# Optimization experiments

Hardware: AMD Instinct MI355X
Metric: run time of the kernel (lower is better)

The kernel has to match this reference:

```python
import jax, jax.numpy as jnp
import numpy as np

B, DIM, H, W = 4, 96, 256, 256
HEADS = 4
EPS = 1e-12

def conv1x1(x, w, b):
    # x: [b,c,h,w], w: [o,c,1,1], b: [o]
    return jnp.einsum('bchw,oc->bohw', x, w[:, :, 0, 0]) + b[None, :, None, None]

def dwconv3x3(x, w, b):
    # depthwise 3x3, w: [c,1,3,3]
    c = x.shape[1]
    y = jax.lax.conv_general_dilated(
        x, w, window_strides=(1, 1), padding='SAME',
        feature_group_count=c, dimension_numbers=('NCHW', 'OIHW', 'NCHW'))
    return y + b[None, :, None, None]

def setup_inputs() -> dict:
    key = jax.random.key(0)
    ks = jax.random.split(key, 16)
    d = DIM
    s = 0.05
    return {
        'content': jax.random.normal(ks[0], (B, d, H, W), jnp.float32),
        'style': jax.random.normal(ks[1], (B, d, H, W), jnp.float32),
        'temperature': jnp.ones((HEADS, 1, 1), jnp.float32),
        'q_w': jax.random.normal(ks[2], (d, d, 1, 1), jnp.float32) * s,
        'q_b': jax.random.normal(ks[3], (d,), jnp.float32) * s,
        'qd_w': jax.random.normal(ks[4], (d, 1, 3, 3), jnp.float32) * s,
        'qd_b': jax.random.normal(ks[5], (d,), jnp.float32) * s,
        'kv_w': jax.random.normal(ks[6], (3 * d, d, 1, 1), jnp.float32) * s,
        'kv_b': jax.random.normal(ks[7], (3 * d,), jnp.float32) * s,
        'kvd_w': jax.random.normal(ks[8], (3 * d, 1, 3, 3), jnp.float32) * s,
        'kvd_b': jax.random.normal(ks[9], (3 * d,), jnp.float32) * s,
        'ps_w': jax.random.normal(ks[10], (d, d, 1, 1), jnp.float32) * s,
        'ps_b': jax.random.normal(ks[11], (d,), jnp.float32) * s,
        'psh_w': jax.random.normal(ks[12], (d, d, 1, 1), jnp.float32) * s,
        'psh_b': jax.random.normal(ks[13], (d,), jnp.float32) * s,
    }

def _heads(x, b, h, w):
    # [b, head*c, h, w] -> [b, head, c, h*w]
    return x.reshape(b, HEADS, x.shape[1] // HEADS, h * w)

def reference(content, style, temperature, q_w, q_b, qd_w, qd_b,
              kv_w, kv_b, kvd_w, kvd_b, ps_w, ps_b, psh_w, psh_b):
    b, c, h, w = content.shape
    kv = dwconv3x3(conv1x1(style, kv_w, kv_b), kvd_w, kvd_b)
    k, v_scale, v_shift = jnp.split(kv, 3, axis=1)
    q = dwconv3x3(conv1x1(content, q_w, q_b), qd_w, qd_b)

    q = _heads(q, b, h, w)
    k = _heads(k, b, h, w)
    v_scale = _heads(v_scale, b, h, w)
    v_shift = _heads(v_shift, b, h, w)

    # L2-normalize over spatial dim (torch F.normalize eps=1e-12)
    q = q / jnp.maximum(jnp.linalg.norm(q, axis=-1, keepdims=True), EPS)
    k = k / jnp.maximum(jnp.linalg.norm(k, axis=-1, keepdims=True), EPS)

    # attn: [b, head, c, c] (channel attention, tiny)
    attn = jnp.einsum('bhcn,bhdn->bhcd', q, k) * temperature[None]
    attn = jax.nn.softmax(attn, axis=-1)

    scale = jnp.einsum('bhcd,bhdn->bhcn', attn, v_scale).reshape(b, c, h, w)
    shift = jnp.einsum('bhcd,bhdn->bhcn', attn, v_shift).reshape(b, c, h, w)

    scale = conv1x1(scale, ps_w, ps_b)
    shift = conv1x1(shift, psh_w, psh_b)
    return (scale, shift)
```

## Files before the change

kernel.cpp:

```cpp
#include <hip/hip_runtime.h>

#define NB 4
#define C 96
#define HH 256
#define WW 256
#define NPIX (HH*WW)
#define HEADS 4
#define CH 24

#define NTX2 16
#define NTY2 19
#define NTILES (NTX2*NTY2)
#define YP 296
#define QP 264
#define VP 104
#define KSPLIT 128
#define YR 24
#define YC 392
#define XTP 76
#define VCH 40

#define WS_SUMSQ_Q 0
#define WS_SUMSQ_K (WS_SUMSQ_Q + NB*C)
#define WS_GRAM    (WS_SUMSQ_K + NB*C)
#define WS_MS      (WS_GRAM + NB*HEADS*CH*CH)
#define WS_MSH     (WS_MS + NB*C*C)

#define XT_OFF_BYTES ((size_t)335872)
#define XT_BYTES   ((size_t)2*NB*NPIX*96*2)

#define F_PSQ_OFF   (XT_OFF_BYTES + XT_BYTES)
#define F_PSQ_BYTES ((size_t)NTILES*NB*192*4)
#define F_PG_OFF    (F_PSQ_OFF + F_PSQ_BYTES)
#define F_PG_BYTES  ((size_t)NTILES*NB*HEADS*1024*4)
#define F_MB_OFF    (F_PG_OFF + F_PG_BYTES)
#define F_MB_BYTES  ((size_t)2*NB*96*96*2)
#define F_WS_NEED   (F_MB_OFF + F_MB_BYTES)

#define QK_OFF    (XT_OFF_BYTES + XT_BYTES)
#define QK_BYTES  ((size_t)2*NB*96*NPIX*2)
#define PG_OFF    (QK_OFF + QK_BYTES)
#define PG_BYTES  ((size_t)KSPLIT*NB*9216*4)
#define PSQ_OFF   (PG_OFF + PG_BYTES)
#define PSQ_BYTES ((size_t)4*NTILES*NB*48*4)
#define MB_OFF    (PSQ_OFF + PSQ_BYTES)
#define MB_BYTES  ((size_t)2*NB*96*96*2)
#define WB_OFF    (MB_OFF + MB_BYTES)
#define WB_BYTES  ((size_t)384*96*2)
#define WS_NEED3  (WB_OFF + WB_BYTES)

typedef short short8 __attribute__((ext_vector_type(8)));
typedef float f32x4 __attribute__((ext_vector_type(4)));
typedef float f32x16 __attribute__((ext_vector_type(16)));

__device__ __forceinline__ unsigned short f2b(float f){
  unsigned u = __float_as_uint(f);
  unsigned r = u + 0x7FFFu + ((u >> 16) & 1u);
  return (unsigned short)(r >> 16);
}
__device__ __forceinline__ float b2f(unsigned short s){
  return __uint_as_float(((unsigned)s) << 16);
}
__device__ __forceinline__ unsigned cvtpk(float lo, float hi){
  unsigned r;
  asm("v_cvt_pk_bf16_f32 %0, %1, %2" : "=v"(r) : "v"(lo), "v"(hi));
  return r;
}
__device__ __forceinline__ short8 pack8(float4 a, float4 b){
  short8 r;
  r[0]=(short)f2b(a.x); r[1]=(short)f2b(a.y); r[2]=(short)f2b(a.z); r[3]=(short)f2b(a.w);
  r[4]=(short)f2b(b.x); r[5]=(short)f2b(b.y); r[6]=(short)f2b(b.z); r[7]=(short)f2b(b.w);
  return r;
}

__global__ __launch_bounds__(256) void k0t(
  const float* __restrict__ content, const float* __restrict__ style,
  unsigned short* __restrict__ xt, int cm)
{
  __shared__ unsigned short Xt[96*XTP];
  const int t = threadIdx.x;
  const int n0 = blockIdx.x * 64;
  const int b = blockIdx.y, src = blockIdx.z;
  const int gyr = n0 >> 8, gxb = n0 & 255;
  const float* in = (src ? style : content) + (size_t)b*C*NPIX;
  #pragma unroll
  for (int i = 0; i < 6; ++i){
    int s = i*256 + t;
    int r = s >> 4, c4 = s & 15;
    float4 f = *(const float4*)(in + (size_t)r*NPIX + n0 + c4*4);
    unsigned lo = ((unsigned)f2b(f.y) << 16) | f2b(f.x);
    unsigned hi = ((unsigned)f2b(f.w) << 16) | f2b(f.z);
    *(uint2*)&Xt[r*XTP + c4*4] = make_uint2(lo, hi);
  }
  __syncthreads();
  unsigned* dst = (unsigned*)(xt + ((size_t)src*NB + b)*NPIX*96);
  #pragma unroll
  for (int i = 0; i < 12; ++i){
    int s = i*256 + t;
    int j = s / 48, c2 = s - j*48;
    unsigned v = ((unsigned)Xt[(c2*2+1)*XTP + j] << 16) | Xt[(c2*2)*XTP + j];
    size_t np = cm ? ((size_t)(gxb + j)*HH + gyr) : (size_t)(n0 + j);
    dst[np*48 + c2] = v;
  }
}

__global__ __launch_bounds__(256) void kwpack(
  const float* __restrict__ q_w, const float* __restrict__ kv_w,
  unsigned short* __restrict__ wb)
{
  int i = blockIdx.x*256 + threadIdx.x;
  if (i < 9216) wb[i] = f2b(q_w[i]);
  else if (i < 36864) wb[i] = f2b(kv_w[i - 9216]);
}

__global__ __launch_bounds__(512, 4) void kconv(
  const unsigned short* __restrict__ xt, const unsigned short* __restrict__ wb,
  const float* __restrict__ q_b, const float* __restrict__ qd_w, const float* __restrict__ qd_b,
  const float* __restrict__ kv_b, const float* __restrict__ kvd_w, const float* __restrict__ kvd_b,
  unsigned short* __restrict__ qk, float* __restrict__ psq)
{
  __shared__ unsigned short Ysh[48*YC];
  __shared__ float red[48];
  const int t = threadIdx.x, lane = t & 63, w = t >> 6;
  const int tile = blockIdx.x, b = blockIdx.y, z = blockIdx.z;
  const int txx = tile & 15, tyy = tile >> 4;
  const int gx0 = txx*16, gy0 = tyy*14;
  const unsigned short* xsrc = xt + ((size_t)((z < 2 ? 0 : 1)*NB + b))*NPIX*96;
  const int wrow0 = (z < 2) ? z*48 : 96 + (z-2)*48;
  const float* cb  = (z<2) ? q_b  + z*48           : kv_b  + (size_t)(z-2)*48;
  const float* dww = (z<2) ? qd_w + (size_t)z*48*9 : kvd_w + (size_t)(z-2)*48*9;
  const float* dwb = (z<2) ? qd_b + z*48           : kvd_b + (size_t)(z-2)*48;
  unsigned short* dst0 = (z < 2)
      ? qk + ((size_t)(0*NB + b)*96 + (size_t)z*48)*NPIX
      : qk + ((size_t)(1*NB + b)*96 + (size_t)(z-2)*48)*NPIX;

  if (t < 48) red[t] = 0.f;

  const int hy = lane & 15, khalf = lane >> 4;
  const int gyh = gy0 - 1 + hy;
  short8 xf[3][3]; bool imv[3];
  const int np = (w < 2) ? 3 : 2;
  #pragma unroll
  for (int i = 0; i < 3; ++i){
    if (i >= np) break;
    int pt = w + i*8;
    int gx = gx0 - 1 + pt;
    bool im = (gx>=0) && (gx<WW) && (gyh>=0) && (gyh<HH);
    imv[i] = im;
    const unsigned short* xp = xsrc + (size_t)(im ? (gx*HH + gyh) : 0)*96 + khalf*8;
    short8 zz = {};
    #pragma unroll
    for (int kk = 0; kk < 3; ++kk){
      short8 v = *(const short8*)(xp + kk*32);
      xf[i][kk] = im ? v : zz;
    }
  }

  #pragma unroll 1
  for (int mi = 0; mi < 3; ++mi){
    const unsigned short* wp = wb + (size_t)(wrow0 + mi*16 + hy)*96 + khalf*8;
    short8 a0 = *(const short8*)(wp);
    short8 a1 = *(const short8*)(wp + 32);
    short8 a2 = *(const short8*)(wp + 64);
    float4 bv = *(const float4*)&cb[mi*16 + khalf*4];
    #pragma unroll
    for (int i = 0; i < 3; ++i){
      if (i >= np) break;
      int pt = w + i*8;
      f32x4 acc = {bv.x, bv.y, bv.z, bv.w};
      acc = __builtin_amdgcn_mfma_f32_16x16x32_bf16(a0, xf[i][0], acc, 0,0,0);
      acc = __builtin_amdgcn_mfma_f32_16x16x32_bf16(a1, xf[i][1], acc, 0,0,0);
      acc = __builtin_amdgcn_mfma_f32_16x16x32_bf16(a2, xf[i][2], acc, 0,0,0);
      #pragma unroll
      for (int r = 0; r < 4; ++r){
        int ch = mi*16 + khalf*4 + r;
        Ysh[ch*YC + hy*YR + pt] = imv[i] ? f2b(acc[r]) : (unsigned short)0;
      }
    }
  }
  __syncthreads();

  for (int sl = lane; sl < 84; sl += 64){
    int slot = w*84 + sl;
    int c = slot / 14, py = slot - (slot/14)*14;
    int gy = gy0 + py;
    if (gy < HH){
      const float* wd = dww + (size_t)c*9;
      float w00=wd[0],w01=wd[1],w02=wd[2],w10=wd[3],w11=wd[4],w12=wd[5],w20=wd[6],w21=wd[7],w22=wd[8];
      float bb = dwb[c];
      const unsigned short* yb = &Ysh[c*YC + py*YR];
      float o[16];
      #pragma unroll
      for (int half = 0; half < 2; ++half){
        float u[3][10];
        #pragma unroll
        for (int uu = 0; uu < 3; ++uu){
          const unsigned short* rp = yb + uu*YR + half*8;
          short8 s = *(const short8*)rp;
          unsigned ex = *(const unsigned*)(rp + 8);
          #pragma unroll
          for (int j = 0; j < 8; ++j) u[uu][j] = b2f((unsigned short)s[j]);
          u[uu][8] = b2f((unsigned short)(ex & 0xffffu));
          u[uu][9] = b2f((unsigned short)(ex >> 16));
        }
        #pragma unroll
        for (int j = 0; j < 8; ++j){
          float s = bb;
          s = fmaf(w00,u[0][j],s); s = fmaf(w01,u[0][j+1],s); s = fmaf(w02,u[0][j+2],s);
          s = fmaf(w10,u[1][j],s); s = fmaf(w11,u[1][j+1],s); s = fmaf(w12,u[1][j+2],s);
          s = fmaf(w20,u[2][j],s); s = fmaf(w21,u[2][j+1],s); s = fmaf(w22,u[2][j+2],s);
          o[half*8 + j] = s;
        }
      }
      float sq = 0.f;
      #pragma unroll
      for (int j = 0; j < 16; ++j) sq = fmaf(o[j], o[j], sq);
      atomicAdd(&red[c], sq);
      unsigned vvp[8];
      #pragma unroll
      for (int jj = 0; jj < 8; ++jj) vvp[jj] = cvtpk(o[2*jj], o[2*jj+1]);
      unsigned short* qp = dst0 + (size_t)c*NPIX + (size_t)gy*WW + gx0;
      *(uint4*)qp       = make_uint4(vvp[0], vvp[1], vvp[2], vvp[3]);
      *(uint4*)(qp + 8) = make_uint4(vvp[4], vvp[5], vvp[6], vvp[7]);
    }
  }
  __syncthreads();
  if (t < 48)
    psq[((size_t)(z*NTILES + tile)*NB + b)*48 + t] = red[t];
}

__global__ __launch_bounds__(384) void kgram(
  const unsigned short* __restrict__ qk, float* __restrict__ pg)
{
  const int t = threadIdx.x, lane = t & 63, wv = t >> 6;
  const int ks = blockIdx.x, b = blockIdx.y;
  const int n0 = ks * (NPIX / KSPLIT);
  const unsigned short* qb = qk + ((size_t)(0*NB + b)*96)*NPIX;
  const unsigned short* kb = qk + ((size_t)(1*NB + b)*96)*NPIX;
  f32x4 acc[6];
  #pragma unroll
  for (int i = 0; i < 6; ++i) acc[i] = (f32x4){0.f,0.f,0.f,0.f};
  #pragma unroll 1
  for (int st = 0; st < (NPIX/KSPLIT)/32; ++st){
    int off = n0 + st*32 + (lane>>4)*8;
    short8 bf = *(const short8*)(kb + (size_t)(wv*16 + (lane&15))*NPIX + off);
    #pragma unroll
    for (int ci = 0; ci < 6; ++ci){
      short8 af = *(const short8*)(qb + (size_t)(ci*16 + (lane&15))*NPIX + off);
      acc[ci] = __builtin_amdgcn_mfma_f32_16x16x32_bf16(af, bf, acc[ci], 0,0,0);
    }
  }
  float* dst = pg + ((size_t)ks*NB + b)*9216;
  #pragma unroll
  for (int ci = 0; ci < 6; ++ci){
    #pragma unroll
    for (int r = 0; r < 4; ++r)
      dst[(ci*6 + wv)*256 + ((lane>>4)*4 + r)*16 + (lane&15)] = acc[ci][r];
  }
}

__global__ __launch_bounds__(256) void kgredN(
  const float* __restrict__ pg, const float* __restrict__ psq, float* __restrict__ ws)
{
  const int b = blockIdx.x, by = blockIdx.y, t = threadIdx.x;
  if (by < 36){
    int ci = by / 6;
    int qrow = ci*16 + (t >> 4), krow = (by - ci*6)*16 + (t & 15);
    float s = 0.f;
    for (int ks = 0; ks < KSPLIT; ++ks)
      s += pg[((size_t)ks*NB + b)*9216 + by*256 + t];
    int h = qrow / CH;
    if (krow / CH == h)
      ws[WS_GRAM + ((size_t)(b*HEADS + h)*CH + (qrow % CH))*CH + (krow % CH)] = s;
  } else {
    if (t < 192){
      int src = t / 96, c = t - (t/96)*96;
      int zz = src*2 + (c/48), cc = c - (c/48)*48;
      float s = 0.f;
      for (int tile = 0; tile < NTILES; ++tile)
        s += psq[((size_t)(zz*NTILES + tile)*NB + b)*48 + cc];
      ws[(src ? WS_SUMSQ_K : WS_SUMSQ_Q) + b*C + c] = s;
    }
  }
}

__global__ void k2_attn(
  const float* __restrict__ temp,
  const float* __restrict__ ps_w, const float* __restrict__ psh_w,
  float* __restrict__ ws, unsigned short* __restrict__ mb)
{
  const int b = blockIdx.x;
  const int t = threadIdx.x;
  __shared__ float attn[C * CH];
  __shared__ float nq[C], nk[C];
  if (t < C){
    nq[t] = fmaxf(sqrtf(ws[WS_SUMSQ_Q + b * C + t]), 1e-12f);
    nk[t] = fmaxf(sqrtf(ws[WS_SUMSQ_K + b * C + t]), 1e-12f);
  }
  __syncthreads();
  if (t < C){
    int h = t / CH;
    const float* g = ws + WS_GRAM + (((size_t)b * HEADS + h) * CH + (t % CH)) * CH;
    float tp = temp[h];
    float row[CH];
    float mx = -3.4e38f;
    #pragma unroll
    for (int d = 0; d < CH; ++d){
      row[d] = g[d] / (nq[t] * nk[h * CH + d]) * tp;
      mx = fmaxf(mx, row[d]);
    }
    float s = 0.f;
    #pragma unroll
    for (int d = 0; d < CH; ++d){ row[d] = expf(row[d] - mx); s += row[d]; }
    float inv = 1.f / s;
    #pragma unroll
    for (int d = 0; d < CH; ++d) attn[t * CH + d] = row[d] * inv;
  }
  __syncthreads();
  for (int idx = t; idx < C * C; idx += 256){
    int o = idx / C, dg = idx - o * C;
    int h = dg / CH, d = dg - h * CH;
    float s1 = 0.f, s2 = 0.f;
    #pragma unroll
    for (int c2 = 0; c2 < CH; ++c2){
      float a = attn[(h * CH + c2) * CH + d];
      s1 = fmaf(ps_w [(size_t)o * C + h * CH + c2], a, s1);
      s2 = fmaf(psh_w[(size_t)o * C + h * CH + c2], a, s2);
    }
    ws[WS_MS  + (size_t)b * C * C + idx] = s1;
    ws[WS_MSH + (size_t)b * C * C + idx] = s2;
    if (mb){
      mb[((size_t)0*NB + b)*9216 + idx] = f2b(s1);
      mb[((size_t)1*NB + b)*9216 + idx] = f2b(s2);
    }
  }
}

__global__ __launch_bounds__(512, 4) void kvm(
  const unsigned short* __restrict__ xt, const unsigned short* __restrict__ wb,
  const float* __restrict__ kv_b, const float* __restrict__ kvd_w, const float* __restrict__ kvd_b,
  const unsigned short* __restrict__ mb,
  const float* __restrict__ ps_b, const float* __restrict__ psh_b,
  float* __restrict__ out)
{
  __shared__ unsigned short Ysh[32*YC];
  __shared__ unsigned short vS[224*VCH];
  const int t = threadIdx.x, lane = t & 63, w = t >> 6;
  const int tile = blockIdx.x, b = blockIdx.y, z = blockIdx.z;
  const int txx = tile & 15, tyy = tile >> 4;
  const int gx0 = txx*16, gy0 = tyy*14;
  const unsigned short* xsrc = xt + ((size_t)(NB + b))*NPIX*96;

  const int hy = lane & 15, khalf = lane >> 4;
  const int gyh = gy0 - 1 + hy;
  short8 xf[3][3]; bool imv[3];
  const int np = (w < 2) ? 3 : 2;
  #pragma unroll
  for (int i = 0; i < 3; ++i){
    if (i >= np) break;
    int pt = w + i*8;
    int gx = gx0 - 1 + pt;
    bool im = (gx>=0) && (gx<WW) && (gyh>=0) && (gyh<HH);
    imv[i] = im;
    const unsigned short* xp = xsrc + (size_t)(im ? (gx*HH + gyh) : 0)*96 + khalf*8;
    short8 zz = {};
    #pragma unroll
    for (int kk = 0; kk < 3; ++kk){
      short8 v = *(const short8*)(xp + kk*32);
      xf[i][kk] = im ? v : zz;
    }
  }

  const float* bias = z ? psh_b : ps_b;
  f32x4 acc[6][2];
  #pragma unroll
  for (int mi = 0; mi < 6; ++mi){
    float4 bv = *(const float4*)&bias[mi*16 + khalf*4];
    acc[mi][0] = (f32x4){bv.x, bv.y, bv.z, bv.w};
    acc[mi][1] = acc[mi][0];
  }
  const unsigned short* mbp = mb + ((size_t)z*NB + b)*9216;

  #pragma unroll 1
  for (int ck = 0; ck < 3; ++ck){
    const int kvrow0 = 96 + z*96 + ck*32;
    #pragma unroll 1
    for (int mi2 = 0; mi2 < 2; ++mi2){
      const unsigned short* wp = wb + (size_t)(96 + kvrow0 + mi2*16 + hy)*96 + khalf*8;
      short8 a0 = *(const short8*)(wp);
      short8 a1 = *(const short8*)(wp + 32);
      short8 a2 = *(const short8*)(wp + 64);
      float4 bv = *(const float4*)&kv_b[kvrow0 + mi2*16 + khalf*4];
      #pragma unroll
      for (int i = 0; i < 3; ++i){
        if (i >= np) break;
        int pt = w + i*8;
        f32x4 a = {bv.x, bv.y, bv.z, bv.w};
        a = __builtin_amdgcn_mfma_f32_16x16x32_bf16(a0, xf[i][0], a, 0,0,0);
        a = __builtin_amdgcn_mfma_f32_16x16x32_bf16(a1, xf[i][1], a, 0,0,0);
        a = __builtin_amdgcn_mfma_f32_16x16x32_bf16(a2, xf[i][2], a, 0,0,0);
        #pragma unroll
        for (int r = 0; r < 4; ++r){
          int ch = mi2*16 + khalf*4 + r;
          Ysh[ch*YC + hy*YR + pt] = imv[i] ? f2b(a[r]) : (unsigned short)0;
        }
      }
    }
    __syncthreads();
    if (t < 448){
      int c2 = t & 31, py = t >> 5;
      const float* wd = kvd_w + (size_t)(kvrow0 + c2)*9;
      float w00=wd[0],w01=wd[1],w02=wd[2],w10=wd[3],w11=wd[4],w12=wd[5],w20=wd[6],w21=wd[7],w22=wd[8];
      float bb = kvd_b[kvrow0 + c2];
      const unsigned short* yb = &Ysh[c2*YC + py*YR];
      float o[16];
      #pragma unroll
      for (int half = 0; half < 2; ++half){
        float u[3][10];
        #pragma unroll
        for (int uu = 0; uu < 3; ++uu){
          const unsigned short* rp = yb + uu*YR + half*8;
          short8 s = *(const short8*)rp;
          unsigned ex = *(const unsigned*)(rp + 8);
          #pragma unroll
          for (int j = 0; j < 8; ++j) u[uu][j] = b2f((unsigned short)s[j]);
          u[uu][8] = b2f((unsigned short)(ex & 0xffffu));
          u[uu][9] = b2f((unsigned short)(ex >> 16));
        }
        #pragma unroll
        for (int j = 0; j < 8; ++j){
          float s = bb;
          s = fmaf(w00,u[0][j],s); s = fmaf(w01,u[0][j+1],s); s = fmaf(w02,u[0][j+2],s);
          s = fmaf(w10,u[1][j],s); s = fmaf(w11,u[1][j+1],s); s = fmaf(w12,u[1][j+2],s);
          s = fmaf(w20,u[2][j],s); s = fmaf(w21,u[2][j+1],s); s = fmaf(w22,u[2][j+2],s);
          o[half*8 + j] = s;
        }
      }
      #pragma unroll
      for (int jj = 0; jj < 8; ++jj){
        unsigned p = cvtpk(o[2*jj], o[2*jj+1]);
        vS[(py*16 + 2*jj    )*VCH + c2] = (unsigned short)p;
        vS[(py*16 + 2*jj + 1)*VCH + c2] = (unsigned short)(p >> 16);
      }
    }
    __syncthreads();
    #pragma unroll
    for (int mi = 0; mi < 6; ++mi){
      short8 a = *(const short8*)(mbp + (size_t)(mi*16 + hy)*96 + ck*32 + khalf*8);
      #pragma unroll
      for (int gi = 0; gi < 2; ++gi){
        int g = w + gi*8;
        if (g < 14){
          short8 bf = *(const short8*)&vS[(size_t)(g*16 + hy)*VCH + khalf*8];
          acc[mi][gi] = __builtin_amdgcn_mfma_f32_16x16x32_bf16(a, bf, acc[mi][gi], 0,0,0);
        }
      }
    }
    __syncthreads();
  }

  float* ob = out + ((size_t)z*NB + b)*(size_t)C*NPIX;
  #pragma unroll
  for (int gi = 0; gi < 2; ++gi){
    int g = w + gi*8;
    int gy = gy0 + g;
    if (g < 14 && gy < HH){
      #pragma unroll
      for (int mi = 0; mi < 6; ++mi){
        #pragma unroll
        for (int r = 0; r < 4; ++r)
          ob[(size_t)(mi*16 + khalf*4 + r)*NPIX + (size_t)gy*WW + gx0 + hy] = acc[mi][gi][r];
      }
    }
  }
}

__device__ __forceinline__ void conv48c(
  const unsigned short* __restrict__ xbase, const float* __restrict__ wmat,
  const float* __restrict__ bias, int row0,
  int gx0, int gy0, int lane, int w, unsigned short* __restrict__ Ysh)
{
  const int hy = lane & 15, khalf = lane >> 4;
  const int gy = gy0 - 1 + hy;
  short8 xf[3][3]; bool imv[3]; int np = (w < 2) ? 3 : 2;
  #pragma unroll
  for (int i = 0; i < 3; ++i){
    if (i >= np) break;
    int pt = w + i*8;
    int gx = gx0 - 1 + pt;
    bool im = (gx>=0) && (gx<WW) && (gy>=0) && (gy<HH);
    imv[i] = im;
    int n = im ? (gy*WW + gx) : 0;
    const unsigned short* xp = xbase + (size_t)n*96 + khalf*8;
    short8 z = {};
    #pragma unroll
    for (int kk = 0; kk < 3; ++kk){
      short8 v = *(const short8*)(xp + kk*32);
      xf[i][kk] = im ? v : z;
    }
  }
  #pragma unroll 1
  for (int mi = 0; mi < 3; ++mi){
    int orow = row0 + mi*16 + hy;
    const float* wp = wmat + (size_t)orow*96 + khalf*8;
    short8 a0 = pack8(*(const float4*)(wp),    *(const float4*)(wp+4));
    short8 a1 = pack8(*(const float4*)(wp+32), *(const float4*)(wp+36));
    short8 a2 = pack8(*(const float4*)(wp+64), *(const float4*)(wp+68));
    float4 bv = *(const float4*)&bias[row0 + mi*16 + khalf*4];
    #pragma unroll
    for (int i = 0; i < 3; ++i){
      if (i >= np) break;
      int pt = w + i*8;
      f32x4 acc = {bv.x, bv.y, bv.z, bv.w};
      acc = __builtin_amdgcn_mfma_f32_16x16x32_bf16(a0, xf[i][0], acc, 0,0,0);
      acc = __builtin_amdgcn_mfma_f32_16x16x32_bf16(a1, xf[i][1], acc, 0,0,0);
      acc = __builtin_amdgcn_mfma_f32_16x16x32_bf16(a2, xf[i][2], acc, 0,0,0);
      #pragma unroll
      for (int r = 0; r < 4; ++r){
        int ch = mi*16 + khalf*4 + r;
        Ysh[ch*YP + pt*16 + hy] = imv[i] ? f2b(acc[r]) : (unsigned short)0;
      }
    }
  }
}

__global__ __launch_bounds__(512, 4) void kqk(
  const unsigned short* __restrict__ xt,
  const float* __restrict__ q_w, const float* __restrict__ q_b,
  const float* __restrict__ qd_w, const float* __restrict__ qd_b,
  const float* __restrict__ kv_w, const float* __restrict__ kv_b,
  const float* __restrict__ kvd_w, const float* __restrict__ kvd_b,
  float* __restrict__ pg, float* __restrict__ psq)
{
  __shared__ unsigned short Ysh[48*YP];
  __shared__ unsigned short qS[48*QP];
  __shared__ unsigned short kT[48*QP];
  __shared__ float redq[C], redk[C];

  const int t = threadIdx.x, lane = t & 63, w = t >> 6;
  const int b = blockIdx.y, tile = blockIdx.x;
  const int txx = tile & 15, tyy = tile >> 4;
  const int gx0 = txx*16, gy0 = tyy*14;
  if (t < C){ redq[t] = 0.f; redk[t] = 0.f; }
  __syncthreads();

  const unsigned short* xc = xt + ((size_t)(0*NB + b))*NPIX*96;
  const unsigned short* xs = xt + ((size_t)(1*NB + b))*NPIX*96;

  auto dwQK = [&](const float* dww, const float* dwb, int wrow0,
                  unsigned short* dst, float* red){
    for (int slot = t; slot < 48*16; slot += 512){
      int c = slot >> 4, j = slot & 15;
      const unsigned short* yb = &Ysh[c*YP + j*16];
      float u0[16], u1[16], u2[16];
      {
        short8 s0 = *(const short8*)(yb),    short8_t_dummy = {};
        short8 s1 = *(const short8*)(yb+8);
        short8 s2 = *(const short8*)(yb+16), s3 = *(const short8*)(yb+24);
        short8 s4 = *(const short8*)(yb+32), s5 = *(const short8*)(yb+40);
        (void)short8_t_dummy;
        #pragma unroll
        for (int u = 0; u < 8; ++u){
          u0[u]=b2f((unsigned short)s0[u]); u0[u+8]=b2f((unsigned short)s1[u]);
          u1[u]=b2f((unsigned short)s2[u]); u1[u+8]=b2f((unsigned short)s3[u]);
          u2[u]=b2f((unsigned short)s4[u]); u2[u+8]=b2f((unsigned short)s5[u]);
        }
      }
      const float* wd = dww + (size_t)(wrow0 + c)*9;
      float w00=wd[0],w01=wd[1],w02=wd[2],w10=wd[3],w11=wd[4],w12=wd[5],w20=wd[6],w21=wd[7],w22=wd[8];
      float bb = dwb[wrow0 + c];
      unsigned short vv[16];
      float sq = 0.f;
      #pragma unroll
      for (int py = 0; py < 14; ++py){
        float s = bb;
        s = fmaf(w00,u0[py],s); s = fmaf(w10,u0[py+1],s); s = fmaf(w20,u0[py+2],s);
        s = fmaf(w01,u1[py],s); s = fmaf(w11,u1[py+1],s); s = fmaf(w21,u1[py+2],s);
        s = fmaf(w02,u2[py],s); s = fmaf(w12,u2[py+1],s); s = fmaf(w22,u2[py+2],s);
        if (gy0 + py >= HH) s = 0.f;
        sq = fmaf(s, s, sq);
        vv[py] = f2b(s);
      }
      vv[14] = 0; vv[15] = 0;
      atomicAdd(&red[wrow0 + c], sq);
      *(short8*)&dst[c*QP + j*16]     = *(short8*)&vv[0];
      *(short8*)&dst[c*QP + j*16 + 8] = *(short8*)&vv[8];
    }
  };

  auto gram = [&](int cc){
    int hl = w & 1, slice = w >> 1;
    int cl = lane & 31; bool cv = cl < CH;
    int row = hl*CH + (cv ? cl : 0);
    f32x16 g;
    #pragma unroll
    for (int r = 0; r < 16; ++r) g[r] = 0.f;
    short8 z = {};
    for (int ks = slice; ks < 16; ks += 4){
      int ko = ks*16 + (lane>>5)*8;
      short8 qa = *(const short8*)&qS[row*QP + ko];
      short8 kb = *(const short8*)&kT[row*QP + ko];
      if (!cv){ qa = z; kb = z; }
      g = __builtin_amdgcn_mfma_f32_32x32x16_bf16(qa, kb, g, 0,0,0);
    }
    float* stg = (float*)Ysh;
    if (slice != 0){
      float* dst = stg + (size_t)(hl*3 + slice - 1)*1024;
      #pragma unroll
      for (int r = 0; r < 16; ++r) dst[r*64 + lane] = g[r];
    }
    __syncthreads();
    if (slice == 0){
      const float* s0 = stg + (size_t)(hl*3 + 0)*1024;
      const float* s1 = stg + (size_t)(hl*3 + 1)*1024;
      const float* s2 = stg + (size_t)(hl*3 + 2)*1024;
      float* dst = pg + ((size_t)(tile*NB + b)*HEADS + cc*2 + hl)*1024;
      #pragma unroll
      for (int r = 0; r < 16; ++r){
        int ix = r*64 + lane;
        dst[ix] = g[r] + s0[ix] + s1[ix] + s2[ix];
      }
    }
  };

  #pragma unroll 1
  for (int cc = 0; cc < 2; ++cc){
    conv48c(xc, q_w, q_b, cc*48, gx0, gy0, lane, w, Ysh);
    __syncthreads();
    dwQK(qd_w, qd_b, cc*48, qS, redq);
    __syncthreads();
    conv48c(xs, kv_w, kv_b, cc*48, gx0, gy0, lane, w, Ysh);
    __syncthreads();
    dwQK(kvd_w, kvd_b, cc*48, kT, redk);
    __syncthreads();
    gram(cc);
    __syncthreads();
  }
  if (t < 192){
    float v = (t < 96) ? redq[t] : redk[t - 96];
    psq[(size_t)(tile*NB + b)*192 + t] = v;
  }
}

__global__ __launch_bounds__(256) void kgredF(
  const float* __restrict__ pg, const float* __restrict__ psq, float* __restrict__ ws)
{
  const int bh = blockIdx.x;
  const int b = bh >> 2, h = bh & 3;
  const int t = threadIdx.x;
  float a0=0.f, a1=0.f, a2=0.f, a3=0.f, sq=0.f;
  for (int tile = 0; tile < NTILES; ++tile){
    const float* p = pg + ((size_t)(tile*NB + b)*HEADS + h)*1024;
    a0 += p[t]; a1 += p[t+256]; a2 += p[t+512]; a3 += p[t+768];
    if (t < 48){
      int ch = h*CH + (t % CH);
      sq += psq[(size_t)(tile*NB + b)*192 + (t < CH ? ch : 96 + ch)];
    }
  }
  if (t < 48){
    if (t < CH) ws[WS_SUMSQ_Q + b*C + h*CH + t] = sq;
    else        ws[WS_SUMSQ_K + b*C + h*CH + (t - CH)] = sq;
  }
  float accs[4] = {a0, a1, a2, a3};
  #pragma unroll
  for (int i = 0; i < 4; ++i){
    int idx = i*256 + t;
    int r = idx >> 6, ln = idx & 63;
    int row = (r&3) + 8*(r>>2) + 4*(ln>>5);
    int col = ln & 31;
    if (row < CH && col < CH)
      ws[WS_GRAM + ((size_t)(b*HEADS + h)*CH + row)*CH + col] = accs[i];
  }
}

__global__ __launch_bounds__(512, 4) void kv_out(
  const unsigned short* __restrict__ xs,
  const float* __restrict__ kv_w, const float* __restrict__ kv_b,
  const float* __restrict__ kvd_w, const float* __restrict__ kvd_b,
  const float* __restrict__ ps_b, const float* __restrict__ psh_b,
  const unsigned short* __restrict__ mb, float* __restrict__ out)
{
  __shared__ unsigned short Ysh[48*YP];
  __shared__ unsigned short vS2[224*VP];
  const int t = threadIdx.x, lane = t & 63, w = t >> 6;
  const int b = blockIdx.y, tile = blockIdx.x;
  const int txx = tile & 15, tyy = tile >> 4;
  const int gx0 = txx*16, gy0 = tyy*14;
  const unsigned short* xb_ = xs + (size_t)b*NPIX*96;

  #pragma unroll 1
  for (int which = 0; which < 2; ++which){
    #pragma unroll 1
    for (int cv = 0; cv < 2; ++cv){
      int row0 = 96 + which*96 + cv*48;
      conv48c(xb_, kv_w, kv_b, row0, gx0, gy0, lane, w, Ysh);
      __syncthreads();
      for (int slot = t; slot < 48*16; slot += 512){
        int c = slot >> 4, j = slot & 15;
        const unsigned short* yb = &Ysh[c*YP + j*16];
        float u0[16], u1[16], u2[16];
        {
          short8 s0 = *(const short8*)(yb),    s1 = *(const short8*)(yb+8);
          short8 s2 = *(const short8*)(yb+16), s3 = *(const short8*)(yb+24);
          short8 s4 = *(const short8*)(yb+32), s5 = *(const short8*)(yb+40);
          #pragma unroll
          for (int u = 0; u < 8; ++u){
            u0[u]=b2f((unsigned short)s0[u]); u0[u+8]=b2f((unsigned short)s1[u]);
            u1[u]=b2f((unsigned short)s2[u]); u1[u+8]=b2f((unsigned short)s3[u]);
            u2[u]=b2f((unsigned short)s4[u]); u2[u+8]=b2f((unsigned short)s5[u]);
          }
        }
        const float* wd = kvd_w + (size_t)(row0 + c)*9;
        float w00=wd[0],w01=wd[1],w02=wd[2],w10=wd[3],w11=wd[4],w12=wd[5],w20=wd[6],w21=wd[7],w22=wd[8];
        float bb = kvd_b[row0 + c];
        #pragma unroll
        for (int py = 0; py < 14; ++py){
          float s = bb;
          s = fmaf(w00,u0[py],s); s = fmaf(w10,u0[py+1],s); s = fmaf(w20,u0[py+2],s);
          s = fmaf(w01,u1[py],s); s = fmaf(w11,u1[py+1],s); s = fmaf(w21,u1[py+2],s);
          s = fmaf(w02,u2[py],s); s = fmaf(w12,u2[py+1],s); s = fmaf(w22,u2[py+2],s);
          vS2[(py*16 + j)*VP + cv*48 + c] = f2b(s);
        }
      }
      __syncthreads();
    }
    const unsigned short* mbp = mb + ((size_t)which*NB + b)*9216;
    const float* bias = which ? psh_b : ps_b;
    float* ob = out + (size_t)which*NB*C*NPIX + (size_t)b*C*NPIX;
    for (int tl = w; tl < 84; tl += 8){
      int mi = tl / 14, n = tl - mi*14;
      const unsigned short* mp = mbp + (size_t)(mi*16 + (lane&15))*96 + (lane>>4)*8;
      short8 a0 = *(const short8*)(mp);
      short8 a1 = *(const short8*)(mp + 32);
      short8 a2 = *(const short8*)(mp + 64);
      float4 bv = *(const float4*)&bias[mi*16 + (lane>>4)*4];
      f32x4 acc = {bv.x, bv.y, bv.z, bv.w};
      const unsigned short* xb = &vS2[(size_t)(n*16 + (lane&15))*VP + (lane>>4)*8];
      acc = __builtin_amdgcn_mfma_f32_16x16x32_bf16(a0, *(const short8*)(xb),    acc, 0,0,0);
      acc = __builtin_amdgcn_mfma_f32_16x16x32_bf16(a1, *(const short8*)(xb+32), acc, 0,0,0);
      acc = __builtin_amdgcn_mfma_f32_16x16x32_bf16(a2, *(const short8*)(xb+64), acc, 0,0,0);
      int gy = gy0 + n;
      if (gy < HH){
        #pragma unroll
        for (int r = 0; r < 4; ++r)
          ob[(size_t)(mi*16 + (lane>>4)*4 + r)*NPIX + gy*WW + gx0 + (lane&15)] = acc[r];
      }
    }
    __syncthreads();
  }
}

extern "C" void kernel_launch(void* const* d_in, const int* in_sizes, int n_in,
                              void* d_out, int out_size, void* d_ws, size_t ws_size,
                              hipStream_t stream)
{
  const float* content = (const float*)d_in[0];
  const float* style   = (const float*)d_in[1];
  const float* temp    = (const float*)d_in[2];
  const float* q_w   = (const float*)d_in[3];
  const float* q_b   = (const float*)d_in[4];
  const float* qd_w  = (const float*)d_in[5];
  const float* qd_b  = (const float*)d_in[6];
  const float* kv_w  = (const float*)d_in[7];
  const float* kv_b  = (const float*)d_in[8];
  const float* kvd_w = (const float*)d_in[9];
  const float* kvd_b = (const float*)d_in[10];
  const float* ps_w  = (const float*)d_in[11];
  const float* ps_b  = (const float*)d_in[12];
  const float* psh_w = (const float*)d_in[13];
  const float* psh_b = (const float*)d_in[14];
  float* out = (float*)d_out;
  float* ws  = (float*)d_ws;

  unsigned short* xt = (unsigned short*)((char*)d_ws + XT_OFF_BYTES);

  if (ws_size >= WS_NEED3){
    unsigned short* qk  = (unsigned short*)((char*)d_ws + QK_OFF);
    float* pg  = (float*)((char*)d_ws + PG_OFF);
    float* psq = (float*)((char*)d_ws + PSQ_OFF);
    unsigned short* mb = (unsigned short*)((char*)d_ws + MB_OFF);
    unsigned short* wb = (unsigned short*)((char*)d_ws + WB_OFF);

    k0t<<<dim3(NPIX/64, NB, 2), dim3(256), 0, stream>>>(content, style, xt, 1);
    kwpack<<<dim3(144), dim3(256), 0, stream>>>(q_w, kv_w, wb);
    kconv<<<dim3(NTILES, NB, 4), dim3(512), 0, stream>>>(
        xt, wb, q_b, qd_w, qd_b, kv_b, kvd_w, kvd_b, qk, psq);
    kgram<<<dim3(KSPLIT, NB), dim3(384), 0, stream>>>(qk, pg);
    kgredN<<<dim3(NB, 37), dim3(256), 0, stream>>>(pg, psq, ws);
    k2_attn<<<dim3(NB), dim3(256), 0, stream>>>(temp, ps_w, psh_w, ws, mb);
    kvm<<<dim3(NTILES, NB, 2), dim3(512), 0, stream>>>(
        xt, wb, kv_b, kvd_w, kvd_b, mb, ps_b, psh_b, out);
  } else {
    float* pg  = (float*)((char*)d_ws + F_PG_OFF);
    float* psq = (float*)((char*)d_ws + F_PSQ_OFF);
    unsigned short* mb = (unsigned short*)((char*)d_ws + F_MB_OFF);
    k0t<<<dim3(NPIX/64, NB, 2), dim3(256), 0, stream>>>(content, style, xt, 0);
    kqk<<<dim3(NTILES, NB), dim3(512), 0, stream>>>(
        xt, q_w, q_b, qd_w, qd_b, kv_w, kv_b, kvd_w, kvd_b, pg, psq);
    kgredF<<<dim3(NB*HEADS), dim3(256), 0, stream>>>(pg, psq, ws);
    k2_attn<<<dim3(NB), dim3(256), 0, stream>>>(temp, ps_w, psh_w, ws, mb);
    kv_out<<<dim3(NTILES, NB), dim3(512), 0, stream>>>(
        xt + (size_t)NB*NPIX*96, kv_w, kv_b, kvd_w, kvd_b, ps_b, psh_b, mb, out);
  }
}
```

Measured before the change: 449.1 us.

## Store q/k in tile-major padded layout and remap blocks across XCDs

kconv now writes q/k intermediates in a tile-contiguous padded layout (224 pixels per tile, zeros for rows outside the image), so each row of 16 pixels lands contiguously and kgram streams a dense padded pixel range with a new split count. Both kconv and kvm also remap the flat block index so consecutive blocks are spread in strides of eight, a swizzle aimed at XCD/L2 locality. The intent is to cut scattered write traffic and improve cache locality, in exchange for a slightly larger qk buffer and gram work over padding pixels.

```diff
diff --git a/kernel.cpp b/kernel.cpp
--- a/kernel.cpp
+++ b/kernel.cpp
@@ -11,6 +11,9 @@
 #define NTX2 16
 #define NTY2 19
 #define NTILES (NTX2*NTY2)
+#define TPX 224
+#define NPIXP (NTILES*TPX)
+#define KSPL2 133
 #define YP 296
 #define QP 264
 #define VP 104
@@ -38,9 +41,9 @@
 #define F_WS_NEED   (F_MB_OFF + F_MB_BYTES)
 
 #define QK_OFF    (XT_OFF_BYTES + XT_BYTES)
-#define QK_BYTES  ((size_t)2*NB*96*NPIX*2)
+#define QK_BYTES  ((size_t)2*NB*96*NPIXP*2)
 #define PG_OFF    (QK_OFF + QK_BYTES)
-#define PG_BYTES  ((size_t)KSPLIT*NB*9216*4)
+#define PG_BYTES  ((size_t)KSPL2*NB*9216*4)
 #define PSQ_OFF   (PG_OFF + PG_BYTES)
 #define PSQ_BYTES ((size_t)4*NTILES*NB*48*4)
 #define MB_OFF    (PSQ_OFF + PSQ_BYTES)
@@ -122,7 +125,9 @@
   __shared__ unsigned short Ysh[48*YC];
   __shared__ float red[48];
   const int t = threadIdx.x, lane = t & 63, w = t >> 6;
-  const int tile = blockIdx.x, b = blockIdx.y, z = blockIdx.z;
+  const int F = blockIdx.x + NTILES*(blockIdx.y + NB*blockIdx.z);
+  const int W = (F & 7)*(NTILES*NB*4/8) + (F >> 3);
+  const int tile = W % NTILES, b = (W / NTILES) % NB, z = W / (NTILES*NB);
   const int txx = tile & 15, tyy = tile >> 4;
   const int gx0 = txx*16, gy0 = tyy*14;
   const unsigned short* xsrc = xt + ((size_t)((z < 2 ? 0 : 1)*NB + b))*NPIX*96;
@@ -131,8 +136,8 @@
   const float* dww = (z<2) ? qd_w + (size_t)z*48*9 : kvd_w + (size_t)(z-2)*48*9;
   const float* dwb = (z<2) ? qd_b + z*48           : kvd_b + (size_t)(z-2)*48;
   unsigned short* dst0 = (z < 2)
-      ? qk + ((size_t)(0*NB + b)*96 + (size_t)z*48)*NPIX
-      : qk + ((size_t)(1*NB + b)*96 + (size_t)(z-2)*48)*NPIX;
+      ? qk + ((size_t)(0*NB + b)*96 + (size_t)z*48)*NPIXP
+      : qk + ((size_t)(1*NB + b)*96 + (size_t)(z-2)*48)*NPIXP;
 
   if (t < 48) red[t] = 0.f;
 
@@ -184,11 +189,236 @@
     int slot = w*84 + sl;
     int c = slot / 14, py = slot - (slot/14)*14;
     int gy = gy0 + py;
-    if (gy < HH){
-      const float* wd = dww + (size_t)c*9;
+    bool valid = (gy < HH);
+    const float* wd = dww + (size_t)c*9;
+    float w00=wd[0],w01=wd[1],w02=wd[2],w10=wd[3],w11=wd[4],w12=wd[5],w20=wd[6],w21=wd[7],w22=wd[8];
+    float bb = dwb[c];
+    const unsigned short* yb = &Ysh[c*YC + py*YR];
+    float o[16];
+    #pragma unroll
+    for (int half = 0; half < 2; ++half){
+      float u[3][10];
+      #pragma unroll
+      for (int uu = 0; uu < 3; ++uu){
+        const unsigned short* rp = yb + uu*YR + half*8;
+        short8 s = *(const short8*)rp;
+        unsigned ex = *(const unsigned*)(rp + 8);
+        #pragma unroll
+        for (int j = 0; j < 8; ++j) u[uu][j] = b2f((unsigned short)s[j]);
+        u[uu][8] = b2f((unsigned short)(ex & 0xffffu));
+        u[uu][9] = b2f((unsigned short)(ex >> 16));
+      }
+      #pragma unroll
+      for (int j = 0; j < 8; ++j){
+        float s = bb;
+        s = fmaf(w00,u[0][j],s); s = fmaf(w01,u[0][j+1],s); s = fmaf(w02,u[0][j+2],s);
+        s = fmaf(w10,u[1][j],s); s = fmaf(w11,u[1][j+1],s); s = fmaf(w12,u[1][j+2],s);
+        s = fmaf(w20,u[2][j],s); s = fmaf(w21,u[2][j+1],s); s = fmaf(w22,u[2][j+2],s);
+        o[half*8 + j] = valid ? s : 0.f;
+      }
+    }
+    float sq = 0.f;
+    #pragma unroll
+    for (int j = 0; j < 16; ++j) sq = fmaf(o[j], o[j], sq);
+    atomicAdd(&red[c], sq);
+    unsigned vvp[8];
+    #pragma unroll
+    for (int jj = 0; jj < 8; ++jj) vvp[jj] = cvtpk(o[2*jj], o[2*jj+1]);
+    unsigned short* qp = dst0 + (size_t)c*NPIXP + tile*TPX + py*16;
+    *(uint4*)qp       = make_uint4(vvp[0], vvp[1], vvp[2], vvp[3]);
+    *(uint4*)(qp + 8) = make_uint4(vvp[4], vvp[5], vvp[6], vvp[7]);
+  }
+  __syncthreads();
+  if (t < 48)
+    psq[((size_t)(z*NTILES + tile)*NB + b)*48 + t] = red[t];
+}
+
+__global__ __launch_bounds__(384) void kgram(
+  const unsigned short* __restrict__ qk, float* __restrict__ pg)
+{
+  const int t = threadIdx.x, lane = t & 63, wv = t >> 6;
+  const int ks = blockIdx.x, b = blockIdx.y;
+  const int n0 = ks * 512;
+  const unsigned short* qb = qk + ((size_t)(0*NB + b)*96)*NPIXP;
+  const unsigned short* kb = qk + ((size_t)(1*NB + b)*96)*NPIXP;
+  f32x4 acc[6];
+  #pragma unroll
+  for (int i = 0; i < 6; ++i) acc[i] = (f32x4){0.f,0.f,0.f,0.f};
+  #pragma unroll 1
+  for (int st = 0; st < 16; ++st){
+    int off = n0 + st*32 + (lane>>4)*8;
+    short8 bf = *(const short8*)(kb + (size_t)(wv*16 + (lane&15))*NPIXP + off);
+    #pragma unroll
+    for (int ci = 0; ci < 6; ++ci){
+      short8 af = *(const short8*)(qb + (size_t)(ci*16 + (lane&15))*NPIXP + off);
+      acc[ci] = __builtin_amdgcn_mfma_f32_16x16x32_bf16(af, bf, acc[ci], 0,0,0);
+    }
+  }
+  float* dst = pg + ((size_t)ks*NB + b)*9216;
+  #pragma unroll
+  for (int ci = 0; ci < 6; ++ci){
+    #pragma unroll
+    for (int r = 0; r < 4; ++r)
+      dst[(ci*6 + wv)*256 + ((lane>>4)*4 + r)*16 + (lane&15)] = acc[ci][r];
+  }
+}
+
+__global__ __launch_bounds__(256) void kgredN(
+  const float* __restrict__ pg, const float* __restrict__ psq, float* __restrict__ ws)
+{
+  const int b = blockIdx.x, by = blockIdx.y, t = threadIdx.x;
+  if (by < 36){
+    int ci = by / 6;
+    int qrow = ci*16 + (t >> 4), krow = (by - ci*6)*16 + (t & 15);
+    float s = 0.f;
+    for (int ks = 0; ks < KSPL2; ++ks)
+      s += pg[((size_t)ks*NB + b)*9216 + by*256 + t];
+    int h = qrow / CH;
+    if (krow / CH == h)
+      ws[WS_GRAM + ((size_t)(b*HEADS + h)*CH + (qrow % CH))*CH + (krow % CH)] = s;
+  } else {
+    if (t < 192){
+      int src = t / 96, c = t - (t/96)*96;
+      int zz = src*2 + (c/48), cc = c - (c/48)*48;
+      float s = 0.f;
+      for (int tile = 0; tile < NTILES; ++tile)
+        s += psq[((size_t)(zz*NTILES + tile)*NB + b)*48 + cc];
+      ws[(src ? WS_SUMSQ_K : WS_SUMSQ_Q) + b*C + c] = s;
+    }
+  }
+}
+
+__global__ void k2_attn(
+  const float* __restrict__ temp,
+  const float* __restrict__ ps_w, const float* __restrict__ psh_w,
+  float* __restrict__ ws, unsigned short* __restrict__ mb)
+{
+  const int b = blockIdx.x;
+  const int t = threadIdx.x;
+  __shared__ float attn[C * CH];
+  __shared__ float nq[C], nk[C];
+  if (t < C){
+    nq[t] = fmaxf(sqrtf(ws[WS_SUMSQ_Q + b * C + t]), 1e-12f);
+    nk[t] = fmaxf(sqrtf(ws[WS_SUMSQ_K + b * C + t]), 1e-12f);
+  }
+  __syncthreads();
+  if (t < C){
+    int h = t / CH;
+    const float* g = ws + WS_GRAM + (((size_t)b * HEADS + h) * CH + (t % CH)) * CH;
+    float tp = temp[h];
+    float row[CH];
+    float mx = -3.4e38f;
+    #pragma unroll
+    for (int d = 0; d < CH; ++d){
+      row[d] = g[d] / (nq[t] * nk[h * CH + d]) * tp;
+      mx = fmaxf(mx, row[d]);
+    }
+    float s = 0.f;
+    #pragma unroll
+    for (int d = 0; d < CH; ++d){ row[d] = expf(row[d] - mx); s += row[d]; }
+    float inv = 1.f / s;
+    #pragma unroll
+    for (int d = 0; d < CH; ++d) attn[t * CH + d] = row[d] * inv;
+  }
+  __syncthreads();
+  for (int idx = t; idx < C * C; idx += 256){
+    int o = idx / C, dg = idx - o * C;
+    int h = dg / CH, d = dg - h * CH;
+    float s1 = 0.f, s2 = 0.f;
+    #pragma unroll
+    for (int c2 = 0; c2 < CH; ++c2){
+      float a = attn[(h * CH + c2) * CH + d];
+      s1 = fmaf(ps_w [(size_t)o * C + h * CH + c2], a, s1);
+      s2 = fmaf(psh_w[(size_t)o * C + h * CH + c2], a, s2);
+    }
+    ws[WS_MS  + (size_t)b * C * C + idx] = s1;
+    ws[WS_MSH + (size_t)b * C * C + idx] = s2;
+    if (mb){
+      mb[((size_t)0*NB + b)*9216 + idx] = f2b(s1);
+      mb[((size_t)1*NB + b)*9216 + idx] = f2b(s2);
+    }
+  }
+}
+
+__global__ __launch_bounds__(512, 4) void kvm(
+  const unsigned short* __restrict__ xt, const unsigned short* __restrict__ wb,
+  const float* __restrict__ kv_b, const float* __restrict__ kvd_w, const float* __restrict__ kvd_b,
+  const unsigned short* __restrict__ mb,
+  const float* __restrict__ ps_b, const float* __restrict__ psh_b,
+  float* __restrict__ out)
+{
+  __shared__ unsigned short Ysh[32*YC];
+  __shared__ unsigned short vS[224*VCH];
+  const int t = threadIdx.x, lane = t & 63, w = t >> 6;
+  const int F = blockIdx.x + NTILES*(blockIdx.y + NB*blockIdx.z);
+  const int W = (F & 7)*(NTILES*NB*2/8) + (F >> 3);
+  const int tile = W % NTILES, b = (W / NTILES) % NB, z = W / (NTILES*NB);
+  const int txx = tile & 15, tyy = tile >> 4;
+  const int gx0 = txx*16, gy0 = tyy*14;
+  const unsigned short* xsrc = xt + ((size_t)(NB + b))*NPIX*96;
+
+  const int hy = lane & 15, khalf = lane >> 4;
+  const int gyh = gy0 - 1 + hy;
+  short8 xf[3][3]; bool imv[3];
+  const int np = (w < 2) ? 3 : 2;
+  #pragma unroll
+  for (int i = 0; i < 3; ++i){
+    if (i >= np) break;
+    int pt = w + i*8;
+    int gx = gx0 - 1 + pt;
+    bool im = (gx>=0) && (gx<WW) && (gyh>=0) && (gyh<HH);
+    imv[i] = im;
+    const unsigned short* xp = xsrc + (size_t)(im ? (gx*HH + gyh) : 0)*96 + khalf*8;
+    short8 zz = {};
+    #pragma unroll
+    for (int kk = 0; kk < 3; ++kk){
+      short8 v = *(const short8*)(xp + kk*32);
+      xf[i][kk] = im ? v : zz;
+    }
+  }
+
+  const float* bias = z ? psh_b : ps_b;
+  f32x4 acc[6][2];
+  #pragma unroll
+  for (int mi = 0; mi < 6; ++mi){
+    float4 bv = *(const float4*)&bias[mi*16 + khalf*4];
+    acc[mi][0] = (f32x4){bv.x, bv.y, bv.z, bv.w};
+    acc[mi][1] = acc[mi][0];
+  }
+  const unsigned short* mbp = mb + ((size_t)z*NB + b)*9216;
+
+  #pragma unroll 1
+  for (int ck = 0; ck < 3; ++ck){
+    const int kvrow0 = 96 + z*96 + ck*32;
+    #pragma unroll 1
+    for (int mi2 = 0; mi2 < 2; ++mi2){
+      const unsigned short* wp = wb + (size_t)(96 + kvrow0 + mi2*16 + hy)*96 + khalf*8;
+      short8 a0 = *(const short8*)(wp);
+      short8 a1 = *(const short8*)(wp + 32);
+      short8 a2 = *(const short8*)(wp + 64);
+      float4 bv = *(const float4*)&kv_b[kvrow0 + mi2*16 + khalf*4];
+      #pragma unroll
+      for (int i = 0; i < 3; ++i){
+        if (i >= np) break;
+        int pt = w + i*8;
+        f32x4 a = {bv.x, bv.y, bv.z, bv.w};
+        a = __builtin_amdgcn_mfma_f32_16x16x32_bf16(a0, xf[i][0], a, 0,0,0);
+        a = __builtin_amdgcn_mfma_f32_16x16x32_bf16(a1, xf[i][1], a, 0,0,0);
+        a = __builtin_amdgcn_mfma_f32_16x16x32_bf16(a2, xf[i][2], a, 0,0,0);
+        #pragma unroll
+        for (int r = 0; r < 4; ++r){
+          int ch = mi2*16 + khalf*4 + r;
+          Ysh[ch*YC + hy*YR + pt] = imv[i] ? f2b(a[r]) : (unsigned short)0;
+        }
+      }
+    }
+    __syncthreads();
+    if (t < 448){
+      int c2 = t & 31, py = t >> 5;
+      const float* wd = kvd_w + (size_t)(kvrow0 + c2)*9;
       float w00=wd[0],w01=wd[1],w02=wd[2],w10=wd[3],w11=wd[4],w12=wd[5],w20=wd[6],w21=wd[7],w22=wd[8];
-      float bb = dwb[c];
-      const unsigned short* yb = &Ysh[c*YC + py*YR];
+      float bb = kvd_b[kvrow0 + c2];
+      const unsigned short* yb = &Ysh[c2*YC + py*YR];
       float o[16];
       #pragma unroll
       for (int half = 0; half < 2; ++half){
@@ -212,230 +442,6 @@
           o[half*8 + j] = s;
         }
       }
-      float sq = 0.f;
-      #pragma unroll
-      for (int j = 0; j < 16; ++j) sq = fmaf(o[j], o[j], sq);
-      atomicAdd(&red[c], sq);
-      unsigned vvp[8];
-      #pragma unroll
-      for (int jj = 0; jj < 8; ++jj) vvp[jj] = cvtpk(o[2*jj], o[2*jj+1]);
-      unsigned short* qp = dst0 + (size_t)c*NPIX + (size_t)gy*WW + gx0;
-      *(uint4*)qp       = make_uint4(vvp[0], vvp[1], vvp[2], vvp[3]);
-      *(uint4*)(qp + 8) = make_uint4(vvp[4], vvp[5], vvp[6], vvp[7]);
-    }
-  }
-  __syncthreads();
-  if (t < 48)
-    psq[((size_t)(z*NTILES + tile)*NB + b)*48 + t] = red[t];
-}
-
-__global__ __launch_bounds__(384) void kgram(
-  const unsigned short* __restrict__ qk, float* __restrict__ pg)
-{
-  const int t = threadIdx.x, lane = t & 63, wv = t >> 6;
-  const int ks = blockIdx.x, b = blockIdx.y;
-  const int n0 = ks * (NPIX / KSPLIT);
-  const unsigned short* qb = qk + ((size_t)(0*NB + b)*96)*NPIX;
-  const unsigned short* kb = qk + ((size_t)(1*NB + b)*96)*NPIX;
-  f32x4 acc[6];
-  #pragma unroll
-  for (int i = 0; i < 6; ++i) acc[i] = (f32x4){0.f,0.f,0.f,0.f};
-  #pragma unroll 1
-  for (int st = 0; st < (NPIX/KSPLIT)/32; ++st){
-    int off = n0 + st*32 + (lane>>4)*8;
-    short8 bf = *(const short8*)(kb + (size_t)(wv*16 + (lane&15))*NPIX + off);
-    #pragma unroll
-    for (int ci = 0; ci < 6; ++ci){
-      short8 af = *(const short8*)(qb + (size_t)(ci*16 + (lane&15))*NPIX + off);
-      acc[ci] = __builtin_amdgcn_mfma_f32_16x16x32_bf16(af, bf, acc[ci], 0,0,0);
-    }
-  }
-  float* dst = pg + ((size_t)ks*NB + b)*9216;
-  #pragma unroll
-  for (int ci = 0; ci < 6; ++ci){
-    #pragma unroll
-    for (int r = 0; r < 4; ++r)
-      dst[(ci*6 + wv)*256 + ((lane>>4)*4 + r)*16 + (lane&15)] = acc[ci][r];
-  }
-}
-
-__global__ __launch_bounds__(256) void kgredN(
-  const float* __restrict__ pg, const float* __restrict__ psq, float* __restrict__ ws)
-{
-  const int b = blockIdx.x, by = blockIdx.y, t = threadIdx.x;
-  if (by < 36){
-    int ci = by / 6;
-    int qrow = ci*16 + (t >> 4), krow = (by - ci*6)*16 + (t & 15);
-    float s = 0.f;
-    for (int ks = 0; ks < KSPLIT; ++ks)
-      s += pg[((size_t)ks*NB + b)*9216 + by*256 + t];
-    int h = qrow / CH;
-    if (krow / CH == h)
-      ws[WS_GRAM + ((size_t)(b*HEADS + h)*CH + (qrow % CH))*CH + (krow % CH)] = s;
-  } else {
-    if (t < 192){
-      int src = t / 96, c = t - (t/96)*96;
-      int zz = src*2 + (c/48), cc = c - (c/48)*48;
-      float s = 0.f;
-      for (int tile = 0; tile < NTILES; ++tile)
-        s += psq[((size_t)(zz*NTILES + tile)*NB + b)*48 + cc];
-      ws[(src ? WS_SUMSQ_K : WS_SUMSQ_Q) + b*C + c] = s;
-    }
-  }
-}
-
-__global__ void k2_attn(
-  const float* __restrict__ temp,
-  const float* __restrict__ ps_w, const float* __restrict__ psh_w,
-  float* __restrict__ ws, unsigned short* __restrict__ mb)
-{
-  const int b = blockIdx.x;
-  const int t = threadIdx.x;
-  __shared__ float attn[C * CH];
-  __shared__ float nq[C], nk[C];
-  if (t < C){
-    nq[t] = fmaxf(sqrtf(ws[WS_SUMSQ_Q + b * C + t]), 1e-12f);
-    nk[t] = fmaxf(sqrtf(ws[WS_SUMSQ_K + b * C + t]), 1e-12f);
-  }
-  __syncthreads();
-  if (t < C){
-    int h = t / CH;
-    const float* g = ws + WS_GRAM + (((size_t)b * HEADS + h) * CH + (t % CH)) * CH;
-    float tp = temp[h];
-    float row[CH];
-    float mx = -3.4e38f;
-    #pragma unroll
-    for (int d = 0; d < CH; ++d){
-      row[d] = g[d] / (nq[t] * nk[h * CH + d]) * tp;
-      mx = fmaxf(mx, row[d]);
-    }
-    float s = 0.f;
-    #pragma unroll
-    for (int d = 0; d < CH; ++d){ row[d] = expf(row[d] - mx); s += row[d]; }
-    float inv = 1.f / s;
-    #pragma unroll
-    for (int d = 0; d < CH; ++d) attn[t * CH + d] = row[d] * inv;
-  }
-  __syncthreads();
-  for (int idx = t; idx < C * C; idx += 256){
-    int o = idx / C, dg = idx - o * C;
-    int h = dg / CH, d = dg - h * CH;
-    float s1 = 0.f, s2 = 0.f;
-    #pragma unroll
-    for (int c2 = 0; c2 < CH; ++c2){
-      float a = attn[(h * CH + c2) * CH + d];
-      s1 = fmaf(ps_w [(size_t)o * C + h * CH + c2], a, s1);
-      s2 = fmaf(psh_w[(size_t)o * C + h * CH + c2], a, s2);
-    }
-    ws[WS_MS  + (size_t)b * C * C + idx] = s1;
-    ws[WS_MSH + (size_t)b * C * C + idx] = s2;
-    if (mb){
-      mb[((size_t)0*NB + b)*9216 + idx] = f2b(s1);
-      mb[((size_t)1*NB + b)*9216 + idx] = f2b(s2);
-    }
-  }
-}
-
-__global__ __launch_bounds__(512, 4) void kvm(
-  const unsigned short* __restrict__ xt, const unsigned short* __restrict__ wb,
-  const float* __restrict__ kv_b, const float* __restrict__ kvd_w, const float* __restrict__ kvd_b,
-  const unsigned short* __restrict__ mb,
-  const float* __restrict__ ps_b, const float* __restrict__ psh_b,
-  float* __restrict__ out)
-{
-  __shared__ unsigned short Ysh[32*YC];
-  __shared__ unsigned short vS[224*VCH];
-  const int t = threadIdx.x, lane = t & 63, w = t >> 6;
-  const int tile = blockIdx.x, b = blockIdx.y, z = blockIdx.z;
-  const int txx = tile & 15, tyy = tile >> 4;
-  const int gx0 = txx*16, gy0 = tyy*14;
-  const unsigned short* xsrc = xt + ((size_t)(NB + b))*NPIX*96;
-
-  const int hy = lane & 15, khalf = lane >> 4;
-  const int gyh = gy0 - 1 + hy;
-  short8 xf[3][3]; bool imv[3];
-  const int np = (w < 2) ? 3 : 2;
-  #pragma unroll
-  for (int i = 0; i < 3; ++i){
-    if (i >= np) break;
-    int pt = w + i*8;
-    int gx = gx0 - 1 + pt;
-    bool im = (gx>=0) && (gx<WW) && (gyh>=0) && (gyh<HH);
-    imv[i] = im;
-    const unsigned short* xp = xsrc + (size_t)(im ? (gx*HH + gyh) : 0)*96 + khalf*8;
-    short8 zz = {};
-    #pragma unroll
-    for (int kk = 0; kk < 3; ++kk){
-      short8 v = *(const short8*)(xp + kk*32);
-      xf[i][kk] = im ? v : zz;
-    }
-  }
-
-  const float* bias = z ? psh_b : ps_b;
-  f32x4 acc[6][2];
-  #pragma unroll
-  for (int mi = 0; mi < 6; ++mi){
-    float4 bv = *(const float4*)&bias[mi*16 + khalf*4];
-    acc[mi][0] = (f32x4){bv.x, bv.y, bv.z, bv.w};
-    acc[mi][1] = acc[mi][0];
-  }
-  const unsigned short* mbp = mb + ((size_t)z*NB + b)*9216;
-
-  #pragma unroll 1
-  for (int ck = 0; ck < 3; ++ck){
-    const int kvrow0 = 96 + z*96 + ck*32;
-    #pragma unroll 1
-    for (int mi2 = 0; mi2 < 2; ++mi2){
-      const unsigned short* wp = wb + (size_t)(96 + kvrow0 + mi2*16 + hy)*96 + khalf*8;
-      short8 a0 = *(const short8*)(wp);
-      short8 a1 = *(const short8*)(wp + 32);
-      short8 a2 = *(const short8*)(wp + 64);
-      float4 bv = *(const float4*)&kv_b[kvrow0 + mi2*16 + khalf*4];
-      #pragma unroll
-      for (int i = 0; i < 3; ++i){
-        if (i >= np) break;
-        int pt = w + i*8;
-        f32x4 a = {bv.x, bv.y, bv.z, bv.w};
-        a = __builtin_amdgcn_mfma_f32_16x16x32_bf16(a0, xf[i][0], a, 0,0,0);
-        a = __builtin_amdgcn_mfma_f32_16x16x32_bf16(a1, xf[i][1], a, 0,0,0);
-        a = __builtin_amdgcn_mfma_f32_16x16x32_bf16(a2, xf[i][2], a, 0,0,0);
-        #pragma unroll
-        for (int r = 0; r < 4; ++r){
-          int ch = mi2*16 + khalf*4 + r;
-          Ysh[ch*YC + hy*YR + pt] = imv[i] ? f2b(a[r]) : (unsigned short)0;
-        }
-      }
-    }
-    __syncthreads();
-    if (t < 448){
-      int c2 = t & 31, py = t >> 5;
-      const float* wd = kvd_w + (size_t)(kvrow0 + c2)*9;
-      float w00=wd[0],w01=wd[1],w02=wd[2],w10=wd[3],w11=wd[4],w12=wd[5],w20=wd[6],w21=wd[7],w22=wd[8];
-      float bb = kvd_b[kvrow0 + c2];
-      const unsigned short* yb = &Ysh[c2*YC + py*YR];
-      float o[16];
-      #pragma unroll
-      for (int half = 0; half < 2; ++half){
-        float u[3][10];
-        #pragma unroll
-        for (int uu = 0; uu < 3; ++uu){
-          const unsigned short* rp = yb + uu*YR + half*8;
-          short8 s = *(const short8*)rp;
-          unsigned ex = *(const unsigned*)(rp + 8);
-          #pragma unroll
-          for (int j = 0; j < 8; ++j) u[uu][j] = b2f((unsigned short)s[j]);
-          u[uu][8] = b2f((unsigned short)(ex & 0xffffu));
-          u[uu][9] = b2f((unsigned short)(ex >> 16));
-        }
-        #pragma unroll
-        for (int j = 0; j < 8; ++j){
-          float s = bb;
-          s = fmaf(w00,u[0][j],s); s = fmaf(w01,u[0][j+1],s); s = fmaf(w02,u[0][j+2],s);
-          s = fmaf(w10,u[1][j],s); s = fmaf(w11,u[1][j+1],s); s = fmaf(w12,u[1][j+2],s);
-          s = fmaf(w20,u[2][j],s); s = fmaf(w21,u[2][j+1],s); s = fmaf(w22,u[2][j+2],s);
-          o[half*8 + j] = s;
-        }
-      }
       #pragma unroll
       for (int jj = 0; jj < 8; ++jj){
         unsigned p = cvtpk(o[2*jj], o[2*jj+1]);
@@ -554,11 +560,10 @@
       const unsigned short* yb = &Ysh[c*YP + j*16];
       float u0[16], u1[16], u2[16];
       {
-        short8 s0 = *(const short8*)(yb),    short8_t_dummy = {};
+        short8 s0 = *(const short8*)(yb);
         short8 s1 = *(const short8*)(yb+8);
         short8 s2 = *(const short8*)(yb+16), s3 = *(const short8*)(yb+24);
         short8 s4 = *(const short8*)(yb+32), s5 = *(const short8*)(yb+40);
-        (void)short8_t_dummy;
         #pragma unroll
         for (int u = 0; u < 8; ++u){
           u0[u]=b2f((unsigned short)s0[u]); u0[u+8]=b2f((unsigned short)s1[u]);
@@ -785,7 +790,7 @@
     kwpack<<<dim3(144), dim3(256), 0, stream>>>(q_w, kv_w, wb);
     kconv<<<dim3(NTILES, NB, 4), dim3(512), 0, stream>>>(
         xt, wb, q_b, qd_w, qd_b, kv_b, kvd_w, kvd_b, qk, psq);
-    kgram<<<dim3(KSPLIT, NB), dim3(384), 0, stream>>>(qk, pg);
+    kgram<<<dim3(KSPL2, NB), dim3(384), 0, stream>>>(qk, pg);
     kgredN<<<dim3(NB, 37), dim3(256), 0, stream>>>(pg, psq, ws);
     k2_attn<<<dim3(NB), dim3(256), 0, stream>>>(temp, ps_w, psh_w, ws, mb);
     kvm<<<dim3(NTILES, NB, 2), dim3(512), 0, stream>>>(
```

Result: slower. 477.2 us (+6.3%).
